# Optimization experiments

Hardware: AMD Instinct MI355X
Metric: run time of the kernel (lower is better)

The kernel has to match this reference:

```python
import jax, jax.numpy as jnp
import numpy as np


def setup_inputs() -> dict:
    key = jax.random.key(0)
    k1, k2, k3 = jax.random.split(key, 3)
    m, h, t, d = 4, 16, 1024, 64
    s = 128  # max_relative_distance
    return {
        "attnQ": jax.random.normal(k1, (m, h, t, d), dtype=jnp.float32),
        "attnK": jax.random.normal(k2, (m, h, t, d), dtype=jnp.float32),
        "pe": jax.random.normal(k3, (2 * s + 1, d), dtype=jnp.float32),
        "max_relative_distance": s,
    }


def reference(attnQ, attnK, pe, max_relative_distance):
    # attnQ: [m, h, t1, d], attnK: [m, h, t2, d] (only t2 is used), pe: [2s+1, d]
    t1 = attnQ.shape[-2]
    t2 = attnK.shape[-2]
    s = max_relative_distance
    # clipped relative distances, shifted into table index range [0, 2s]
    rel = jnp.arange(t1)[:, None] - jnp.arange(t2)[None, :]          # [t1, t2]
    rel = jnp.clip(rel, -s, s) + min(s + 1, max(t1, t2)) - 1         # [t1, t2]
    emb = pe[rel]                                                    # [t1, t2, d]
    emb = jnp.transpose(emb, (0, 2, 1))                              # [t1, d, t2]
    # per-query-position matmul of Q rows against relative embeddings
    return jnp.einsum('mhtd,tds->mhts', attnQ, emb)                  # [m, h, t1, t2]
```

## Files before the change

kernel.cpp:

```cpp
#include <hip/hip_runtime.h>
#include <stdint.h>
#include <stddef.h>

#define T_LEN 1024
#define D_DIM 64
#define NPE   257
#define BI    16
#define QP_ST 266
#define NT    4

typedef _Float16 h16;
typedef h16   h16x8 __attribute__((ext_vector_type(8)));
typedef float f32x4 __attribute__((ext_vector_type(4)));

__device__ __forceinline__ unsigned short f2h_bits(float f) {
    union { h16 h; unsigned short u; } c; c.h = (h16)f; return c.u;
}
__device__ __forceinline__ float lo_h(uint32_t p) {
    union { uint32_t u; h16 h[2]; } c; c.u = p; return (float)c.h[0];
}
__device__ __forceinline__ float hi_h(uint32_t p) {
    union { uint32_t u; h16 h[2]; } c; c.u = p; return (float)c.h[1];
}
__device__ __forceinline__ float4 ld4(const float* p) {
    return *reinterpret_cast<const float4*>(p);
}
__device__ __forceinline__ h16x8 cvt8h(float4 a, float4 b) {
    h16x8 r;
    r[0] = (h16)a.x; r[1] = (h16)a.y; r[2] = (h16)a.z; r[3] = (h16)a.w;
    r[4] = (h16)b.x; r[5] = (h16)b.y; r[6] = (h16)b.z; r[7] = (h16)b.w;
    return r;
}

#define SPLIT1(hi, lo, idx, val)                      \
    { const float _v = (val); const h16 _h = (h16)_v; \
      hi[idx] = _h; lo[idx] = (h16)(_v - (float)_h); }

__global__ __launch_bounds__(256, 4)
void relpos_fused(const float* __restrict__ Q,
                  const float* __restrict__ pe,
                  float* __restrict__ out) {
    __shared__ unsigned short qp_s[2][BI][QP_ST];

    const int tid   = threadIdx.x;
    const int mh    = blockIdx.x;
    const int by    = blockIdx.y;
    const int wave  = tid >> 6;
    const int lane  = tid & 63;
    const int row16 = lane & 15;
    const int kgrp  = lane >> 4;

#define PE_LOAD(N, B0, B1)                                                     \
    h16x8 B0, B1;                                                              \
    {                                                                          \
        const float* prow = pe + (size_t)(wave * 64 + (N) * 16 + row16) * D_DIM \
                               + kgrp * 8;                                     \
        B0 = cvt8h(ld4(prow),      ld4(prow + 4));                             \
        B1 = cvt8h(ld4(prow + 32), ld4(prow + 36));                            \
    }
    PE_LOAD(0, pb0_0, pb1_0)
    PE_LOAD(1, pb0_1, pb1_1)
    PE_LOAD(2, pb0_2, pb1_2)
    PE_LOAD(3, pb0_3, pb1_3)
    h16x8 pb0_t16, pb1_t16;
    if (wave == 3) {
        const float* prow = pe + (size_t)256 * D_DIM + kgrp * 8;
        pb0_t16 = cvt8h(ld4(prow),      ld4(prow + 4));
        pb1_t16 = cvt8h(ld4(prow + 32), ld4(prow + 36));
    }

    float4 nqa, nqb, nqc, nqd;
#define QLOAD(IT)                                                              \
    {                                                                          \
        const float* qrow = Q + ((size_t)mh * T_LEN + (IT) * BI + row16) * D_DIM \
                              + kgrp * 8;                                      \
        nqa = ld4(qrow);      nqb = ld4(qrow + 4);                             \
        nqc = ld4(qrow + 32); nqd = ld4(qrow + 36);                            \
    }

#define TILE(N, B0, B1, BUF)                                                   \
    {                                                                          \
        f32x4 acc = {0.f, 0.f, 0.f, 0.f};                                      \
        acc = __builtin_amdgcn_mfma_f32_16x16x32_f16(a0h, B0, acc, 0, 0, 0);   \
        acc = __builtin_amdgcn_mfma_f32_16x16x32_f16(a1h, B1, acc, 0, 0, 0);   \
        acc = __builtin_amdgcn_mfma_f32_16x16x32_f16(a0l, B0, acc, 0, 0, 0);   \
        acc = __builtin_amdgcn_mfma_f32_16x16x32_f16(a1l, B1, acc, 0, 0, 0);   \
        const int cb = wave * 64 + (N) * 16;                                   \
        qp_s[BUF][kgrp * 4 + 0][4 + cb + row16] = f2h_bits(acc[0]);            \
        qp_s[BUF][kgrp * 4 + 1][4 + cb + row16] = f2h_bits(acc[1]);            \
        qp_s[BUF][kgrp * 4 + 2][4 + cb + row16] = f2h_bits(acc[2]);            \
        qp_s[BUF][kgrp * 4 + 3][4 + cb + row16] = f2h_bits(acc[3]);            \
        if ((N) == 0 && wave == 0 && row16 == 0) {                             \
            _Pragma("unroll")                                                  \
            for (int j = 0; j < 4; ++j) {                                      \
                const unsigned short v = f2h_bits(acc[j]);                     \
                unsigned short* qr = &qp_s[BUF][kgrp * 4 + j][0];              \
                qr[0] = v; qr[1] = v; qr[2] = v; qr[3] = v;                    \
            }                                                                  \
        }                                                                      \
    }

#define BCOMPUTE(BUF)                                                          \
    {                                                                          \
        h16x8 a0h, a0l, a1h, a1l;                                             \
        SPLIT1(a0h, a0l, 0, nqa.x) SPLIT1(a0h, a0l, 1, nqa.y)                 \
        SPLIT1(a0h, a0l, 2, nqa.z) SPLIT1(a0h, a0l, 3, nqa.w)                 \
        SPLIT1(a0h, a0l, 4, nqb.x) SPLIT1(a0h, a0l, 5, nqb.y)                 \
        SPLIT1(a0h, a0l, 6, nqb.z) SPLIT1(a0h, a0l, 7, nqb.w)                 \
        SPLIT1(a1h, a1l, 0, nqc.x) SPLIT1(a1h, a1l, 1, nqc.y)                 \
        SPLIT1(a1h, a1l, 2, nqc.z) SPLIT1(a1h, a1l, 3, nqc.w)                 \
        SPLIT1(a1h, a1l, 4, nqd.x) SPLIT1(a1h, a1l, 5, nqd.y)                 \
        SPLIT1(a1h, a1l, 6, nqd.z) SPLIT1(a1h, a1l, 7, nqd.w)                 \
        TILE(0, pb0_0, pb1_0, BUF)                                             \
        TILE(1, pb0_1, pb1_1, BUF)                                             \
        TILE(2, pb0_2, pb1_2, BUF)                                             \
        TILE(3, pb0_3, pb1_3, BUF)                                             \
        if (wave == 3) {                \
            f32x4 acc = {0.f, 0.f, 0.f, 0.f};                                  \
            acc = __builtin_amdgcn_mfma_f32_16x16x32_f16(a0h, pb0_t16, acc, 0, 0, 0); \
            acc = __builtin_amdgcn_mfma_f32_16x16x32_f16(a1h, pb1_t16, acc, 0, 0, 0); \
            acc = __builtin_amdgcn_mfma_f32_16x16x32_f16(a0l, pb0_t16, acc, 0, 0, 0); \
            acc = __builtin_amdgcn_mfma_f32_16x16x32_f16(a1l, pb1_t16, acc, 0, 0, 0); \
            if (row16 == 0) {                                                  \
                _Pragma("unroll")                                              \
                for (int j = 0; j < 4; ++j) {                                  \
                    const unsigned short v = f2h_bits(acc[j]);                 \
                    unsigned short* qr = &qp_s[BUF][kgrp * 4 + j][0];          \
                    qr[260] = v; qr[261] = v; qr[262] = v;                     \
                    qr[263] = v; qr[264] = v;                                  \
                }                                                              \
            }                                                                  \
        }                                                                      \
    }

    QLOAD(by * NT)
    BCOMPUTE(0)

    const int j0 = tid << 2;
#pragma unroll
    for (int t = 0; t < NT; ++t) {
        __syncthreads();
        if (t + 1 < NT) { QLOAD(by * NT + t + 1) }

        {
            const int it = by * NT + t;
            float4* dst = reinterpret_cast<float4*>(
                              out + ((size_t)mh * T_LEN + it * BI) * T_LEN) + tid;
#pragma unroll 4
            for (int r = 0; r < BI; ++r) {
                const int i = it * BI + r;
                int cbs = i - j0 + 125;
                cbs = cbs < -4 ? -4 : (cbs > 257 ? 257 : cbs);
                const int s = cbs + 4;
                const uint32_t* row =
                    reinterpret_cast<const uint32_t*>(&qp_s[t & 1][r][0]);
                const int d0 = s >> 1;
                const uint32_t w0 = row[d0], w1 = row[d0 + 1], w2 = row[d0 + 2];
                const uint32_t sh = (uint32_t)(s & 1) << 4;
                const uint32_t p01 = __builtin_amdgcn_alignbit(w1, w0, sh);
                const uint32_t p23 = __builtin_amdgcn_alignbit(w2, w1, sh);
                float4 v;
                v.x = hi_h(p23);
                v.y = lo_h(p23);
                v.z = hi_h(p01);
                v.w = lo_h(p01);
                *dst = v;
                dst += T_LEN / 4;
            }
        }

        if (t + 1 < NT) { BCOMPUTE((t + 1) & 1) }
    }
}

extern "C" void kernel_launch(void* const* d_in, const int* in_sizes, int n_in,
                              void* d_out, int out_size, void* d_ws, size_t ws_size,
                              hipStream_t stream) {
    const float* Q  = (const float*)d_in[0];
    const float* pe = (const float*)d_in[2];
    float* out = (float*)d_out;

    const int mh = in_sizes[0] / (T_LEN * D_DIM);
    dim3 grid(mh, (T_LEN / BI) / NT);
    relpos_fused<<<grid, 256, 0, stream>>>(Q, pe, out);
}
```

Baseline: 59.78 us.

## Store QP table as reversed fp32 rows for aligned vector LDS reads

The shared-memory QP table now holds fp32 values in reversed column order, padded so that each output row reads its four consecutive outputs with one aligned 16-byte LDS load. This replaces the three 32-bit loads, alignbit shifts and fp16-to-fp32 conversions per output float4. Output writes become nontemporal stores. The cost is double the LDS footprint and more scalar edge-replication stores. The table also no longer rounds values to fp16, which improves precision.

```diff
diff --git a/kernel.cpp b/kernel.cpp
--- a/kernel.cpp
+++ b/kernel.cpp
@@ -4,24 +4,15 @@
 
 #define T_LEN 1024
 #define D_DIM 64
-#define NPE   257
 #define BI    16
-#define QP_ST 266
 #define NT    4
+#define QP_DW 276
 
 typedef _Float16 h16;
 typedef h16   h16x8 __attribute__((ext_vector_type(8)));
 typedef float f32x4 __attribute__((ext_vector_type(4)));
+typedef float vfloat4 __attribute__((ext_vector_type(4)));
 
-__device__ __forceinline__ unsigned short f2h_bits(float f) {
-    union { h16 h; unsigned short u; } c; c.h = (h16)f; return c.u;
-}
-__device__ __forceinline__ float lo_h(uint32_t p) {
-    union { uint32_t u; h16 h[2]; } c; c.u = p; return (float)c.h[0];
-}
-__device__ __forceinline__ float hi_h(uint32_t p) {
-    union { uint32_t u; h16 h[2]; } c; c.u = p; return (float)c.h[1];
-}
 __device__ __forceinline__ float4 ld4(const float* p) {
     return *reinterpret_cast<const float4*>(p);
 }
@@ -40,7 +31,7 @@
 void relpos_fused(const float* __restrict__ Q,
                   const float* __restrict__ pe,
                   float* __restrict__ out) {
-    __shared__ unsigned short qp_s[2][BI][QP_ST];
+    __shared__ float qp_s[2][BI][QP_DW];
 
     const int tid   = threadIdx.x;
     const int mh    = blockIdx.x;
@@ -85,18 +76,16 @@
         acc = __builtin_amdgcn_mfma_f32_16x16x32_f16(a1h, B1, acc, 0, 0, 0);   \
         acc = __builtin_amdgcn_mfma_f32_16x16x32_f16(a0l, B0, acc, 0, 0, 0);   \
         acc = __builtin_amdgcn_mfma_f32_16x16x32_f16(a1l, B1, acc, 0, 0, 0);   \
-        const int cb = wave * 64 + (N) * 16;                                   \
-        qp_s[BUF][kgrp * 4 + 0][4 + cb + row16] = f2h_bits(acc[0]);            \
-        qp_s[BUF][kgrp * 4 + 1][4 + cb + row16] = f2h_bits(acc[1]);            \
-        qp_s[BUF][kgrp * 4 + 2][4 + cb + row16] = f2h_bits(acc[2]);            \
-        qp_s[BUF][kgrp * 4 + 3][4 + cb + row16] = f2h_bits(acc[3]);            \
-        if ((N) == 0 && wave == 0 && row16 == 0) {                             \
+        const int col = wave * 64 + (N) * 16 + row16;                          \
+        qp_s[BUF][kgrp * 4 + 0][264 + 0 - col] = acc[0];                       \
+        qp_s[BUF][kgrp * 4 + 1][264 + 1 - col] = acc[1];                       \
+        qp_s[BUF][kgrp * 4 + 2][264 + 2 - col] = acc[2];                       \
+        qp_s[BUF][kgrp * 4 + 3][264 + 3 - col] = acc[3];                       \
+        if ((N) == 0 && wave == 0 && row16 == 0) {         \
             _Pragma("unroll")                                                  \
-            for (int j = 0; j < 4; ++j) {                                      \
-                const unsigned short v = f2h_bits(acc[j]);                     \
-                unsigned short* qr = &qp_s[BUF][kgrp * 4 + j][0];              \
-                qr[0] = v; qr[1] = v; qr[2] = v; qr[3] = v;                    \
-            }                                                                  \
+            for (int j = 0; j < 4; ++j)                                        \
+                for (int d = 265 + j; d < 272; ++d)                            \
+                    qp_s[BUF][kgrp * 4 + j][d] = acc[j];                       \
         }                                                                      \
     }
 
@@ -115,19 +104,18 @@
         TILE(1, pb0_1, pb1_1, BUF)                                             \
         TILE(2, pb0_2, pb1_2, BUF)                                             \
         TILE(3, pb0_3, pb1_3, BUF)                                             \
-        if (wave == 3) {                \
+        if (wave == 3) {      \
             f32x4 acc = {0.f, 0.f, 0.f, 0.f};                                  \
             acc = __builtin_amdgcn_mfma_f32_16x16x32_f16(a0h, pb0_t16, acc, 0, 0, 0); \
             acc = __builtin_amdgcn_mfma_f32_16x16x32_f16(a1h, pb1_t16, acc, 0, 0, 0); \
             acc = __builtin_amdgcn_mfma_f32_16x16x32_f16(a0l, pb0_t16, acc, 0, 0, 0); \
             acc = __builtin_amdgcn_mfma_f32_16x16x32_f16(a1l, pb1_t16, acc, 0, 0, 0); \
-            if (row16 == 0) {                                                  \
+            if (row16 == 0) {       \
                 _Pragma("unroll")                                              \
                 for (int j = 0; j < 4; ++j) {                                  \
-                    const unsigned short v = f2h_bits(acc[j]);                 \
-                    unsigned short* qr = &qp_s[BUF][kgrp * 4 + j][0];          \
-                    qr[260] = v; qr[261] = v; qr[262] = v;                     \
-                    qr[263] = v; qr[264] = v;                                  \
+                    qp_s[BUF][kgrp * 4 + j][8 + j] = acc[j];                   \
+                    for (int d = 0; d < 8 + j; ++d)                            \
+                        qp_s[BUF][kgrp * 4 + j][d] = acc[j];                   \
                 }                                                              \
             }                                                                  \
         }                                                                      \
@@ -143,29 +131,20 @@
         if (t + 1 < NT) { QLOAD(by * NT + t + 1) }
 
         {
-            const int it = by * NT + t;
-            float4* dst = reinterpret_cast<float4*>(
-                              out + ((size_t)mh * T_LEN + it * BI) * T_LEN) + tid;
+            const int it  = by * NT + t;
+            const int i0t = it * BI;
+            float* dstf = out + ((size_t)mh * T_LEN + i0t) * T_LEN + j0;
+            const float* qb = &qp_s[t & 1][0][0];
 #pragma unroll 4
             for (int r = 0; r < BI; ++r) {
-                const int i = it * BI + r;
-                int cbs = i - j0 + 125;
-                cbs = cbs < -4 ? -4 : (cbs > 257 ? 257 : cbs);
-                const int s = cbs + 4;
-                const uint32_t* row =
-                    reinterpret_cast<const uint32_t*>(&qp_s[t & 1][r][0]);
-                const int d0 = s >> 1;
-                const uint32_t w0 = row[d0], w1 = row[d0 + 1], w2 = row[d0 + 2];
-                const uint32_t sh = (uint32_t)(s & 1) << 4;
-                const uint32_t p01 = __builtin_amdgcn_alignbit(w1, w0, sh);
-                const uint32_t p23 = __builtin_amdgcn_alignbit(w2, w1, sh);
-                float4 v;
-                v.x = hi_h(p23);
-                v.y = lo_h(p23);
-                v.z = hi_h(p01);
-                v.w = lo_h(p01);
-                *dst = v;
-                dst += T_LEN / 4;
+                const int i  = i0t + r;
+                const int A  = i - 128 - (r & 3);
+                int jc = j0 < A - 8 ? A - 8 : j0;
+                jc = jc > A + 260 ? A + 260 : jc;
+                const float* src = qb + r * QP_DW + (jc - A + 8);
+                const vfloat4 v = *reinterpret_cast<const vfloat4*>(src);
+                __builtin_nontemporal_store(v, reinterpret_cast<vfloat4*>(dstf));
+                dstf += T_LEN;
             }
         }
 
```

After: 63.52 us. 1.06x slower.
